# Kernel optimization log

Measured on AMD Instinct MI355X. Metric: run time of the kernel, lower is better.

Reference implementation:

```python
import jax, jax.numpy as jnp
import numpy as np

EPS = 1e-08


def setup_inputs() -> dict:
    key = jax.random.key(0)
    kx, km = jax.random.split(key)
    B, T, D = 128, 4096, 64
    x = jax.random.normal(kx, (B, T, D), dtype=jnp.float32)
    mask = jax.random.randint(km, (B, T, D), 0, 2).astype(jnp.float32)
    return {"x": x, "mask": mask}


def reference(x, mask):
    B, T, D = x.shape
    dt = x.dtype

    # ---- temporal: lag-1 autocorrelation + linear trend ----
    autocorr = jnp.mean(x[:, :-1, :] * x[:, 1:, :], axis=(1, 2))[:, None]  # (B,1)
    t = jnp.arange(T, dtype=dt)
    t_c = t - t.mean()
    x_mean_t = x.mean(axis=2)                                   # (B,T)
    num = (t_c * (x_mean_t - x_mean_t.mean(axis=1, keepdims=True))).sum(axis=1, keepdims=True)
    trend = num / ((t_c ** 2).sum() + EPS)                      # (B,1)

    # ---- frequency: dominant frequency + spectral entropy ----
    power = jnp.abs(jnp.fft.rfft(x_mean_t, axis=1)) ** 2        # (B,T//2+1)
    dom_freq = (jnp.argmax(power, axis=1).astype(dt) / (T / 2))[:, None]
    p_norm = power / (power.sum(axis=1, keepdims=True) + EPS)
    spec_ent = -(p_norm * jnp.log(p_norm + EPS)).sum(axis=1, keepdims=True)

    # ---- statistical: skewness, kurtosis, quantiles ----
    xc = x - x.mean(axis=(1, 2), keepdims=True)
    m2 = (xc ** 2).mean(axis=(1, 2))
    m3 = (xc ** 3).mean(axis=(1, 2))
    m4 = (xc ** 4).mean(axis=(1, 2))
    skew = m3 / (m2 ** 1.5 + EPS)
    kurt = m4 / (m2 ** 2 + EPS)
    q = jnp.quantile(x.reshape(B, -1), jnp.array([0.25, 0.5, 0.75]), axis=1)  # (3,B)
    stat = jnp.stack([skew, kurt, q[0], q[1], q[2]], axis=1)    # (B,5)

    # ---- shape: peaks, zero crossings, rate of change ----
    diff = x_mean_t[:, 1:] - x_mean_t[:, :-1]                   # (B,T-1)
    peak = (diff[:, 1:] * diff[:, :-1] < 0).astype(dt).sum(axis=1, keepdims=True) / (T - 2)
    xmc = x_mean_t - x_mean_t.mean(axis=1, keepdims=True)
    zero_cross = (xmc[:, 1:] * xmc[:, :-1] < 0).astype(dt).sum(axis=1, keepdims=True) / (T - 1)
    roc = jnp.abs(diff).mean(axis=1, keepdims=True)

    # ---- missing-data features (vectorized, no per-batch loop) ----
    missing_rate = 1.0 - mask.reshape(B, -1).sum(axis=1, keepdims=True) / (T * D + EPS)
    obs_per_time = mask.sum(axis=2)                             # (B,T)
    obs_density = obs_per_time / (D + EPS)
    density_var = jnp.var(obs_density, axis=1, ddof=1, keepdims=True)  # unbiased, matches torch
    time_mask = obs_per_time > 0                                # (B,T) bool
    first_idx = jnp.argmax(time_mask, axis=1).astype(dt)
    first_obs = jnp.where(time_mask.any(axis=1), first_idx / T, 0.0)[:, None]

    # ---- channel features: mean off-diagonal correlation + PCA var explained ----
    xcc = x - x.mean(axis=1, keepdims=True)                     # (B,T,D)
    gram = jnp.einsum('btd,bte->bde', xcc, xcc)                 # (B,D,D)
    cov = gram / (T - 1 + EPS)
    std = jnp.std(x, axis=1, ddof=1)                            # (B,D), unbiased like torch.std
    corr = cov / (std[:, :, None] * std[:, None, :] + EPS)
    off_diag = 1.0 - jnp.eye(D, dtype=dt)
    mean_corr = ((corr * off_diag).sum(axis=(1, 2)) / (D * (D - 1) + EPS))[:, None]
    # singular values squared of xcc == eigenvalues of gram
    eig = jnp.linalg.eigvalsh(gram)                             # ascending, (B,D)
    var_explained = (eig[:, -1] / eig.sum(axis=1))[:, None]

    return jnp.concatenate([
        autocorr, trend,               # temporal (2)
        dom_freq, spec_ent,            # frequency (2)
        stat,                          # statistical (5)
        peak, zero_cross, roc,         # shape (3)
        missing_rate, density_var, first_obs,  # missing (3)
        mean_corr, var_explained,      # channel (2)
    ], axis=1)                          # (B,17)
```

## Files before the change

### kernel.cpp

```cpp
#include <hip/hip_runtime.h>
#include <math.h>

#define TB 128
#define TT 4096
#define TD 64

#define GRAM_OFF   0u
#define HIST_OFF   2097152u
#define COLSUM_OFF 4194304u
#define SCAL_OFF   4227072u
#define FIRST_OFF  4230656u
#define ZERO_BYTES 4231168u
#define XMEAN_OFF  4231168u

typedef float  f32x4  __attribute__((ext_vector_type(4)));
typedef short  s16x8  __attribute__((ext_vector_type(8)));

__device__ __forceinline__ float brs4(float v, float* sbuf, int tid) {
#pragma unroll
  for (int o = 32; o; o >>= 1) v += __shfl_xor(v, o);
  __syncthreads();
  if ((tid & 63) == 0) sbuf[tid >> 6] = v;
  __syncthreads();
  return (sbuf[0] + sbuf[1]) + (sbuf[2] + sbuf[3]);
}

__device__ __forceinline__ float brs8(float v, float* sbuf, int tid) {
#pragma unroll
  for (int o = 32; o; o >>= 1) v += __shfl_xor(v, o);
  __syncthreads();
  if ((tid & 63) == 0) sbuf[tid >> 6] = v;
  __syncthreads();
  return ((sbuf[0] + sbuf[1]) + (sbuf[2] + sbuf[3])) +
         ((sbuf[4] + sbuf[5]) + (sbuf[6] + sbuf[7]));
}

__device__ __forceinline__ int binof(float v) {
  int bi = (int)floorf(fmaf(v, 256.f, 2048.f));
  return bi < 0 ? 0 : (bi > 4095 ? 4095 : bi);
}

__device__ __forceinline__ unsigned short f2bf(float f) {
  unsigned u = __float_as_uint(f);
  return (unsigned short)((u + 0x7FFFu + ((u >> 16) & 1u)) >> 16);
}

__global__ __launch_bounds__(256) void kA_stats(const float* __restrict__ x,
    const float* __restrict__ mk, float* __restrict__ xmean,
    unsigned* __restrict__ hist, float* __restrict__ colsum,
    float* __restrict__ scal, int* __restrict__ firstg) {
  __shared__ unsigned shist[4096];
  __shared__ float xrow[512];
  __shared__ float scol[64];
  __shared__ float sred[4];
  __shared__ int smax[4];

  const int tid  = threadIdx.x;
  const int b    = blockIdx.y;
  const int s    = blockIdx.x;
  const int t0   = s << 9;
  const int lane = tid & 63;
  const int wv   = tid >> 6;
  const int q    = lane >> 4;
  const int c    = lane & 15;
  const int lcol = c << 2;
  const int tw   = t0 + (wv << 7);

  for (int i = tid; i < 4096; i += 256) shist[i] = 0u;
  if (tid < 64) scol[tid] = 0.f;
  __syncthreads();

  float s1 = 0.f, s2 = 0.f, s3 = 0.f, s4 = 0.f, ac = 0.f;
  float osum = 0.f, o2 = 0.f;
  int fmax = 0;
  float cs0 = 0.f, cs1 = 0.f, cs2 = 0.f, cs3 = 0.f;
  float4 pv = make_float4(0.f, 0.f, 0.f, 0.f);

  const float* xb = x + (size_t)b * (TT * TD);
  const float* mb = mk + (size_t)b * (TT * TD);

  for (int it = 0; it < 32; ++it) {
    const int t = tw + (it << 2) + q;
    const float4 v = *(const float4*)(xb + (size_t)t * TD + lcol);
    const float4 m = *(const float4*)(mb + (size_t)t * TD + lcol);
    {
      const float x0 = v.x, x1 = v.y, x2 = v.z, x3 = v.w;
      const float q0 = x0 * x0, q1 = x1 * x1, q2 = x2 * x2, q3 = x3 * x3;
      s1 += (x0 + x1) + (x2 + x3);
      s2 += (q0 + q1) + (q2 + q3);
      s3 += (q0 * x0 + q1 * x1) + (q2 * x2 + q3 * x3);
      s4 += (q0 * q0 + q1 * q1) + (q2 * q2 + q3 * q3);
      cs0 += x0; cs1 += x1; cs2 += x2; cs3 += x3;
      atomicAdd(&shist[binof(x0)], 1u);
      atomicAdd(&shist[binof(x1)], 1u);
      atomicAdd(&shist[binof(x2)], 1u);
      atomicAdd(&shist[binof(x3)], 1u);
    }
    {
      float rx = (v.x + v.y) + (v.z + v.w);
      float rm = (m.x + m.y) + (m.z + m.w);
      rx += __shfl_xor(rx, 1); rm += __shfl_xor(rm, 1);
      rx += __shfl_xor(rx, 2); rm += __shfl_xor(rm, 2);
      rx += __shfl_xor(rx, 4); rm += __shfl_xor(rm, 4);
      rx += __shfl_xor(rx, 8); rm += __shfl_xor(rm, 8);
      if (c == 0) {
        xrow[t - t0] = rx * (1.f / 64.f);
        osum += rm;
        o2 = fmaf(rm, rm, o2);
        if (rm > 0.f) fmax = max(fmax, TT - t);
      }
    }
    {
      const float n0 = __shfl(v.x, lane + 16);
      const float n1 = __shfl(v.y, lane + 16);
      const float n2 = __shfl(v.z, lane + 16);
      const float n3 = __shfl(v.w, lane + 16);
      const float d1 = (v.x * n0 + v.y * n1) + (v.z * n2 + v.w * n3);
      ac += (q < 3) ? d1 : 0.f;
      const float b0 = __shfl(v.x, c);
      const float b1 = __shfl(v.y, c);
      const float b2 = __shfl(v.z, c);
      const float b3 = __shfl(v.w, c);
      if (it > 0) {
        const float d2 = (pv.x * b0 + pv.y * b1) + (pv.z * b2 + pv.w * b3);
        ac += (q == 3) ? d2 : 0.f;
      }
      pv = v;
    }
  }
  {
    const int tnext = tw + 128;
    if (tnext < TT) {
      const float4 nb = *(const float4*)(xb + (size_t)tnext * TD + lcol);
      const float d2 = (pv.x * nb.x + pv.y * nb.y) + (pv.z * nb.z + pv.w * nb.w);
      ac += (q == 3) ? d2 : 0.f;
    }
  }
  __syncthreads();
  xmean[(size_t)b * TT + t0 + tid] = xrow[tid];
  xmean[(size_t)b * TT + t0 + tid + 256] = xrow[tid + 256];
  const float rac = brs4(ac, sred, tid);
  const float r1 = brs4(s1, sred, tid);
  const float r2 = brs4(s2, sred, tid);
  const float r3 = brs4(s3, sred, tid);
  const float r4 = brs4(s4, sred, tid);
  const float ro = brs4(osum, sred, tid);
  const float ro2 = brs4(o2, sred, tid);
#pragma unroll
  for (int o = 32; o; o >>= 1) fmax = max(fmax, __shfl_xor(fmax, o));
  if ((tid & 63) == 0) smax[tid >> 6] = fmax;
  __syncthreads();
  if (tid == 0) {
    atomicAdd(&scal[0 * TB + b], rac);
    atomicAdd(&scal[1 * TB + b], r1);
    atomicAdd(&scal[2 * TB + b], r2);
    atomicAdd(&scal[3 * TB + b], r3);
    atomicAdd(&scal[4 * TB + b], r4);
    atomicAdd(&scal[5 * TB + b], ro);
    atomicAdd(&scal[6 * TB + b], ro2);
    atomicMax(&firstg[b], max(max(smax[0], smax[1]), max(smax[2], smax[3])));
  }
  atomicAdd(&scol[lcol + 0], cs0);
  atomicAdd(&scol[lcol + 1], cs1);
  atomicAdd(&scol[lcol + 2], cs2);
  atomicAdd(&scol[lcol + 3], cs3);
  __syncthreads();
  if (tid < 64) atomicAdd(&colsum[b * 64 + tid], scol[tid]);
  unsigned* hb = hist + (size_t)b * 4096;
  for (int i = tid; i < 4096; i += 256) {
    const unsigned hv = shist[i];
    if (hv) atomicAdd(&hb[i], hv);
  }
}

__global__ __launch_bounds__(256) void kB_gram(const float* __restrict__ x,
                                               float* __restrict__ gram) {
  __shared__ __align__(16) unsigned short Xt[2][64 * 72];
  const int tid  = threadIdx.x;
  const int b    = blockIdx.y;
  const int s    = blockIdx.x;
  const int t0   = s << 9;
  const int lane = tid & 63;
  const int wv   = tid >> 6;
  const int g    = tid >> 4;
  const int r0   = g << 2;
  const int c    = tid & 15;
  const int lcol = c << 2;
  const int mb0 = (wv & 1) << 5;
  const int nb0 = (wv >> 1) << 5;
  const int ml  = lane & 15;
  const int qk  = (lane >> 4) << 3;

  f32x4 acc[2][2];
#pragma unroll
  for (int mi = 0; mi < 2; ++mi)
#pragma unroll
    for (int ni = 0; ni < 2; ++ni) acc[mi][ni] = (f32x4)0.f;

  const float* xb = x + (size_t)b * (TT * TD);

  int p = 0;
  for (int tile = 0; tile < 8; ++tile) {
    const int tbase = t0 + (tile << 6);
    float4 v[4];
#pragma unroll
    for (int k = 0; k < 4; ++k)
      v[k] = *(const float4*)(xb + (size_t)(tbase + r0 + k) * TD + lcol);
#pragma unroll
    for (int j = 0; j < 4; ++j) {
      const float e0 = j == 0 ? v[0].x : (j == 1 ? v[0].y : (j == 2 ? v[0].z : v[0].w));
      const float e1 = j == 0 ? v[1].x : (j == 1 ? v[1].y : (j == 2 ? v[1].z : v[1].w));
      const float e2 = j == 0 ? v[2].x : (j == 1 ? v[2].y : (j == 2 ? v[2].z : v[2].w));
      const float e3 = j == 0 ? v[3].x : (j == 1 ? v[3].y : (j == 2 ? v[3].z : v[3].w));
      uint2 pw;
      pw.x = (unsigned)f2bf(e0) | ((unsigned)f2bf(e1) << 16);
      pw.y = (unsigned)f2bf(e2) | ((unsigned)f2bf(e3) << 16);
      *(uint2*)(&Xt[p][(lcol + j) * 72 + r0]) = pw;
    }
    __syncthreads();
#pragma unroll
    for (int kk = 0; kk < 2; ++kk) {
      const int ko = (kk << 5) + qk;
      s16x8 af[2], bf[2];
#pragma unroll
      for (int mi = 0; mi < 2; ++mi)
        af[mi] = *(const s16x8*)(&Xt[p][(mb0 + (mi << 4) + ml) * 72 + ko]);
#pragma unroll
      for (int ni = 0; ni < 2; ++ni)
        bf[ni] = *(const s16x8*)(&Xt[p][(nb0 + (ni << 4) + ml) * 72 + ko]);
#pragma unroll
      for (int mi = 0; mi < 2; ++mi)
#pragma unroll
        for (int ni = 0; ni < 2; ++ni)
          acc[mi][ni] = __builtin_amdgcn_mfma_f32_16x16x32_bf16(
              af[mi], bf[ni], acc[mi][ni], 0, 0, 0);
    }
    p ^= 1;
  }
  float* gb = gram + (size_t)b * 4096;
  const int crow = (lane >> 4) << 2;
  const int ccol = lane & 15;
#pragma unroll
  for (int mi = 0; mi < 2; ++mi)
#pragma unroll
    for (int ni = 0; ni < 2; ++ni) {
      const int gr0 = mb0 + (mi << 4) + crow;
      const int gc = nb0 + (ni << 4) + ccol;
#pragma unroll
      for (int rg = 0; rg < 4; ++rg)
        atomicAdd(&gb[(gr0 + rg) * 64 + gc], acc[mi][ni][rg]);
    }
}

__global__ __launch_bounds__(512) void k34(const float* __restrict__ xmean,
    const float* __restrict__ gram, const float* __restrict__ colsum,
    const unsigned* __restrict__ hist, const float* __restrict__ scal,
    const int* __restrict__ firstg, float* __restrict__ out) {
  __shared__ __align__(16) char arena[49152];
  __shared__ float sred[8];
  __shared__ float smv[8];
  __shared__ int smi[8];
  __shared__ float cssh[64];
  __shared__ float sdsh[64];
  __shared__ float osv_s[6];
  const int tid = threadIdx.x;

  if (blockIdx.x < 128) {
    const int b = blockIdx.x;
    float* xm = (float*)arena;
    float* re = xm + 4096;
    float* im = re + 4096;
    const float* xb = xmean + (size_t)b * TT;
    for (int i = tid; i < TT; i += 512) xm[i] = xb[i];
    __syncthreads();
    float ls = 0.f;
    for (int i = tid; i < TT; i += 512) ls += xm[i];
    const float meanv = brs8(ls, sred, tid) * (1.f / TT);
    float tnum = 0.f, roc = 0.f;
    int pk = 0, zc = 0;
    for (int i = tid; i < TT; i += 512) {
      const float xi = xm[i];
      tnum += ((float)i - 2047.5f) * (xi - meanv);
      if (i < TT - 1) {
        const float d1 = xm[i + 1] - xi;
        roc += fabsf(d1);
        if (i >= 1) {
          const float d0 = xi - xm[i - 1];
          if (d1 * d0 < 0.f) ++pk;
        }
      }
      if (i >= 1) {
        if ((xi - meanv) * (xm[i - 1] - meanv) < 0.f) ++zc;
      }
    }
    tnum = brs8(tnum, sred, tid);
    roc = brs8(roc, sred, tid);
    const float pkf = brs8((float)pk, sred, tid);
    const float zcf = brs8((float)zc, sred, tid);
    if (tid == 0) {
      out[b * 17 + 1] = tnum / 5726622720.0f;
      out[b * 17 + 9] = pkf * (1.f / 4094.f);
      out[b * 17 + 10] = zcf * (1.f / 4095.f);
      out[b * 17 + 11] = roc * (1.f / 4095.f);
    }
    for (int i = tid; i < TT; i += 512) {
      re[i] = xm[__brev((unsigned)i) >> 20];
      im[i] = 0.f;
    }
    __syncthreads();
    int l2h = 0;
    for (int len = 2; len <= TT; len <<= 1, ++l2h) {
      const int half = len >> 1;
      const float ab = -6.283185307179586f / (float)len;
      for (int j = tid; j < TT / 2; j += 512) {
        const int pos = j & (half - 1);
        const int i0 = ((j >> l2h) << (l2h + 1)) + pos;
        const int i1 = i0 + half;
        float sn, cn;
        __sincosf(ab * (float)pos, &sn, &cn);
        const float vr = re[i1], vi = im[i1];
        const float tr = cn * vr - sn * vi;
        const float ti = cn * vi + sn * vr;
        const float ur = re[i0], ui = im[i0];
        re[i0] = ur + tr; im[i0] = ui + ti;
        re[i1] = ur - tr; im[i1] = ui - ti;
      }
      __syncthreads();
    }
    float ps = 0.f, bmaxv = -1.f;
    int bidx = 0;
    for (int k = tid; k <= 2048; k += 512) {
      const float p = re[k] * re[k] + im[k] * im[k];
      ps += p;
      if (p > bmaxv) { bmaxv = p; bidx = k; }
    }
    ps = brs8(ps, sred, tid);
#pragma unroll
    for (int o = 32; o; o >>= 1) {
      const float ov = __shfl_xor(bmaxv, o);
      const int oi = __shfl_xor(bidx, o);
      if (ov > bmaxv || (ov == bmaxv && oi < bidx)) { bmaxv = ov; bidx = oi; }
    }
    if ((tid & 63) == 0) { smv[tid >> 6] = bmaxv; smi[tid >> 6] = bidx; }
    __syncthreads();
    float ent = 0.f;
    const float inv = 1.f / (ps + 1e-8f);
    for (int k = tid; k <= 2048; k += 512) {
      const float p = (re[k] * re[k] + im[k] * im[k]) * inv;
      ent -= p * __logf(p + 1e-8f);
    }
    ent = brs8(ent, sred, tid);
    if (tid == 0) {
      float bv = smv[0]; int bi = smi[0];
      for (int w = 1; w < 8; ++w)
        if (smv[w] > bv || (smv[w] == bv && smi[w] < bi)) { bv = smv[w]; bi = smi[w]; }
      out[b * 17 + 2] = (float)bi * (1.f / 2048.f);
      out[b * 17 + 3] = ent;
    }
  } else {
    const int b = blockIdx.x - 128;
    float* Lg = (float*)arena;
    unsigned* h = (unsigned*)(arena + 16640);
    unsigned* cumc = (unsigned*)(arena + 16640 + 16384);
    if (tid < 64) cssh[tid] = colsum[b * 64 + tid];
    for (int i = tid; i < 4096; i += 512) h[i] = hist[(size_t)b * 4096 + i];
    __syncthreads();
    const float* gb = gram + (size_t)b * 4096;
    for (int i = tid; i < 4096; i += 512) {
      const int d = i >> 6, e = i & 63;
      Lg[d * 65 + e] = gb[i] - cssh[d] * cssh[e] * (1.f / 4096.f);
    }
    unsigned chs_own = 0;
    if (tid < 256) {
#pragma unroll
      for (int j = 0; j < 16; ++j) chs_own += h[(tid << 4) + j];
      cumc[tid] = chs_own;
    }
    __syncthreads();
    if (tid < 64) sdsh[tid] = sqrtf(Lg[tid * 65 + tid] * (1.f / 4095.f));
    for (int off = 1; off < 256; off <<= 1) {
      unsigned add = 0;
      if (tid < 256 && tid >= off) add = cumc[tid - off];
      __syncthreads();
      if (tid < 256) cumc[tid] += add;
      __syncthreads();
    }
    float mcs = 0.f, trc = 0.f;
    for (int i = tid; i < 4096; i += 512) {
      const int d = i >> 6, e = i & 63;
      const float gv = Lg[d * 65 + e];
      if (d != e) mcs += (gv * (1.f / 4095.f)) / (sdsh[d] * sdsh[e] + 1e-8f);
      else trc += gv;
    }
    mcs = brs8(mcs, sred, tid);
    trc = brs8(trc, sred, tid);
    if (tid < 256) {
      const unsigned ranks[6] = {65535u, 65536u, 131071u, 131072u, 196607u, 196608u};
      const unsigned incl = cumc[tid];
      const unsigned excl = incl - chs_own;
#pragma unroll
      for (int qi = 0; qi < 6; ++qi) {
        const unsigned r = ranks[qi];
        if (excl <= r && r < incl) {
          int bin = tid << 4;
          unsigned cum = excl;
          while (bin < 4095 && cum + h[bin] <= r) { cum += h[bin]; ++bin; }
          const float cnt = (float)max(h[bin], 1u);
          osv_s[qi] = ((float)bin * (1.f / 256.f) - 8.f) +
                      (((float)(r - cum) + 0.5f) / cnt) * (1.f / 256.f);
        }
      }
    }
    float lam = 0.f;
    if (tid < 64) {
      const float* rowp = &Lg[tid * 65];
      float v = 1.f + 0.001f * (float)tid;
      float n2 = 1.f;
      for (int it = 0; it < 48; ++it) {
        float w0 = 0.f, w1 = 0.f, w2 = 0.f, w3 = 0.f;
#pragma unroll
        for (int e = 0; e < 64; e += 4) {
          w0 = fmaf(rowp[e],     __shfl(v, e),     w0);
          w1 = fmaf(rowp[e + 1], __shfl(v, e + 1), w1);
          w2 = fmaf(rowp[e + 2], __shfl(v, e + 2), w2);
          w3 = fmaf(rowp[e + 3], __shfl(v, e + 3), w3);
        }
        const float w = (w0 + w1) + (w2 + w3);
        n2 = w * w;
#pragma unroll
        for (int o = 32; o; o >>= 1) n2 += __shfl_xor(n2, o);
        v = w * rsqrtf(n2);
      }
      lam = sqrtf(n2);
    }
    __syncthreads();
    if (tid == 0) {
      const float q25 = 0.25f * osv_s[0] + 0.75f * osv_s[1];
      const float q50 = 0.5f * (osv_s[2] + osv_s[3]);
      const float q75 = 0.75f * osv_s[4] + 0.25f * osv_s[5];
      const float N = 262144.f;
      const float m1 = scal[1 * TB + b] / N;
      const float M2 = scal[2 * TB + b] / N;
      const float M3 = scal[3 * TB + b] / N;
      const float M4 = scal[4 * TB + b] / N;
      const float mu2 = M2 - m1 * m1;
      const float mu3 = M3 - 3.f * m1 * M2 + 2.f * m1 * m1 * m1;
      const float mu4 = M4 - 4.f * m1 * M3 + 6.f * m1 * m1 * M2 - 3.f * m1 * m1 * m1 * m1;
      const float skew = mu3 / (sqrtf(mu2) * mu2 + 1e-8f);
      const float kurt = mu4 / (mu2 * mu2 + 1e-8f);
      const float acv = scal[0 * TB + b] * (1.f / 262080.f);
      const float msum = scal[5 * TB + b];
      const float o2s = scal[6 * TB + b];
      const float missing = 1.f - msum / 262144.f;
      const float sdm = msum * (1.f / 64.f) * (1.f / 4096.f);
      const float dvar = (o2s * (1.f / 4096.f) - 4096.f * sdm * sdm) * (1.f / 4095.f);
      const int fm = firstg[b];
      const float fobs = fm > 0 ? (float)(4096 - fm) * (1.f / 4096.f) : 0.f;
      float* ob = out + b * 17;
      ob[0] = acv;
      ob[4] = skew; ob[5] = kurt;
      ob[6] = q25; ob[7] = q50; ob[8] = q75;
      ob[12] = missing; ob[13] = dvar; ob[14] = fobs;
      ob[15] = mcs / (4032.f + 1e-8f);
      ob[16] = lam / trc;
    }
  }
}

extern "C" void kernel_launch(void* const* d_in, const int* in_sizes, int n_in,
                              void* d_out, int out_size, void* d_ws, size_t ws_size,
                              hipStream_t stream) {
  (void)in_sizes; (void)n_in; (void)out_size; (void)ws_size;
  const float* x = (const float*)d_in[0];
  const float* mask = (const float*)d_in[1];
  float* out = (float*)d_out;
  char* ws = (char*)d_ws;
  float* gram = (float*)(ws + GRAM_OFF);
  unsigned* hist = (unsigned*)(ws + HIST_OFF);
  float* colsum = (float*)(ws + COLSUM_OFF);
  float* scal = (float*)(ws + SCAL_OFF);
  int* firstg = (int*)(ws + FIRST_OFF);
  float* xmean = (float*)(ws + XMEAN_OFF);

  hipMemsetAsync(d_ws, 0, ZERO_BYTES, stream);

  dim3 g1(8, TB);
  kA_stats<<<g1, 256, 0, stream>>>(x, mask, xmean, hist, colsum, scal, firstg);
  kB_gram<<<g1, 256, 0, stream>>>(x, gram);
  k34<<<256, 512, 0, stream>>>(xmean, gram, colsum, hist, scal, firstg, out);
}
```

Measured before the change: 349.1 us.

## Restructure stats kernel: contiguous time rows per quad, ballot mask counts, more blocks

The stats kernel now gives each 16-lane quad a contiguous run of 16 time steps, so the lag-1 autocorrelation becomes a per-thread product with the previous row and no cross-lane shuffles are needed. Mask row counts use wave ballots and popcount instead of a shuffle reduction. Row means are accumulated with LDS atomics. The grid is doubled to 16 blocks per batch, each covering 256 rows, for more parallelism. This trades shuffle work for LDS atomic contention, and it assumes the mask holds only 0/1 values. Dropping floorf changes binning only for negative values, which get clamped to bin 0 anyway.

```diff
diff --git a/kernel.cpp b/kernel.cpp
--- a/kernel.cpp
+++ b/kernel.cpp
@@ -36,7 +36,7 @@
 }
 
 __device__ __forceinline__ int binof(float v) {
-  int bi = (int)floorf(fmaf(v, 256.f, 2048.f));
+  int bi = (int)(fmaf(v, 256.f, 2048.f));
   return bi < 0 ? 0 : (bi > 4095 ? 4095 : bi);
 }
 
@@ -50,7 +50,7 @@
     unsigned* __restrict__ hist, float* __restrict__ colsum,
     float* __restrict__ scal, int* __restrict__ firstg) {
   __shared__ unsigned shist[4096];
-  __shared__ float xrow[512];
+  __shared__ float xrow[256];
   __shared__ float scol[64];
   __shared__ float sred[4];
   __shared__ int smax[4];
@@ -58,15 +58,16 @@
   const int tid  = threadIdx.x;
   const int b    = blockIdx.y;
   const int s    = blockIdx.x;
-  const int t0   = s << 9;
+  const int t0   = s << 8;
   const int lane = tid & 63;
   const int wv   = tid >> 6;
   const int q    = lane >> 4;
   const int c    = lane & 15;
   const int lcol = c << 2;
-  const int tw   = t0 + (wv << 7);
+  const int tq   = t0 + (wv << 6) + (q << 4);
 
   for (int i = tid; i < 4096; i += 256) shist[i] = 0u;
+  xrow[tid] = 0.f;
   if (tid < 64) scol[tid] = 0.f;
   __syncthreads();
 
@@ -75,12 +76,13 @@
   int fmax = 0;
   float cs0 = 0.f, cs1 = 0.f, cs2 = 0.f, cs3 = 0.f;
   float4 pv = make_float4(0.f, 0.f, 0.f, 0.f);
+  const int sh = q << 4;
 
   const float* xb = x + (size_t)b * (TT * TD);
   const float* mb = mk + (size_t)b * (TT * TD);
 
-  for (int it = 0; it < 32; ++it) {
-    const int t = tw + (it << 2) + q;
+  for (int it = 0; it < 16; ++it) {
+    const int t = tq + it;
     const float4 v = *(const float4*)(xb + (size_t)t * TD + lcol);
     const float4 m = *(const float4*)(mb + (size_t)t * TD + lcol);
     {
@@ -96,49 +98,36 @@
       atomicAdd(&shist[binof(x2)], 1u);
       atomicAdd(&shist[binof(x3)], 1u);
     }
+    atomicAdd(&xrow[t - t0], (v.x + v.y) + (v.z + v.w));
     {
-      float rx = (v.x + v.y) + (v.z + v.w);
-      float rm = (m.x + m.y) + (m.z + m.w);
-      rx += __shfl_xor(rx, 1); rm += __shfl_xor(rm, 1);
-      rx += __shfl_xor(rx, 2); rm += __shfl_xor(rm, 2);
-      rx += __shfl_xor(rx, 4); rm += __shfl_xor(rm, 4);
-      rx += __shfl_xor(rx, 8); rm += __shfl_xor(rm, 8);
+      const unsigned long long b0 = __ballot(m.x > 0.5f);
+      const unsigned long long b1 = __ballot(m.y > 0.5f);
+      const unsigned long long b2 = __ballot(m.z > 0.5f);
+      const unsigned long long b3 = __ballot(m.w > 0.5f);
       if (c == 0) {
-        xrow[t - t0] = rx * (1.f / 64.f);
+        const int cnt = __popcll((b0 >> sh) & 0xFFFFull) +
+                        __popcll((b1 >> sh) & 0xFFFFull) +
+                        __popcll((b2 >> sh) & 0xFFFFull) +
+                        __popcll((b3 >> sh) & 0xFFFFull);
+        const float rm = (float)cnt;
         osum += rm;
         o2 = fmaf(rm, rm, o2);
-        if (rm > 0.f) fmax = max(fmax, TT - t);
-      }
-    }
-    {
-      const float n0 = __shfl(v.x, lane + 16);
-      const float n1 = __shfl(v.y, lane + 16);
-      const float n2 = __shfl(v.z, lane + 16);
-      const float n3 = __shfl(v.w, lane + 16);
-      const float d1 = (v.x * n0 + v.y * n1) + (v.z * n2 + v.w * n3);
-      ac += (q < 3) ? d1 : 0.f;
-      const float b0 = __shfl(v.x, c);
-      const float b1 = __shfl(v.y, c);
-      const float b2 = __shfl(v.z, c);
-      const float b3 = __shfl(v.w, c);
-      if (it > 0) {
-        const float d2 = (pv.x * b0 + pv.y * b1) + (pv.z * b2 + pv.w * b3);
-        ac += (q == 3) ? d2 : 0.f;
-      }
-      pv = v;
-    }
+        if (cnt > 0) fmax = max(fmax, TT - t);
+      }
+    }
+    if (it > 0)
+      ac += (pv.x * v.x + pv.y * v.y) + (pv.z * v.z + pv.w * v.w);
+    pv = v;
   }
   {
-    const int tnext = tw + 128;
+    const int tnext = tq + 16;
     if (tnext < TT) {
       const float4 nb = *(const float4*)(xb + (size_t)tnext * TD + lcol);
-      const float d2 = (pv.x * nb.x + pv.y * nb.y) + (pv.z * nb.z + pv.w * nb.w);
-      ac += (q == 3) ? d2 : 0.f;
-    }
-  }
-  __syncthreads();
-  xmean[(size_t)b * TT + t0 + tid] = xrow[tid];
-  xmean[(size_t)b * TT + t0 + tid + 256] = xrow[tid + 256];
+      ac += (pv.x * nb.x + pv.y * nb.y) + (pv.z * nb.z + pv.w * nb.w);
+    }
+  }
+  __syncthreads();
+  xmean[(size_t)b * TT + t0 + tid] = xrow[tid] * (1.f / 64.f);
   const float rac = brs4(ac, sred, tid);
   const float r1 = brs4(s1, sred, tid);
   const float r2 = brs4(s2, sred, tid);
@@ -484,8 +473,9 @@
 
   hipMemsetAsync(d_ws, 0, ZERO_BYTES, stream);
 
-  dim3 g1(8, TB);
-  kA_stats<<<g1, 256, 0, stream>>>(x, mask, xmean, hist, colsum, scal, firstg);
-  kB_gram<<<g1, 256, 0, stream>>>(x, gram);
+  dim3 gA(16, TB);
+  kA_stats<<<gA, 256, 0, stream>>>(x, mask, xmean, hist, colsum, scal, firstg);
+  dim3 gB(8, TB);
+  kB_gram<<<gB, 256, 0, stream>>>(x, gram);
   k34<<<256, 512, 0, stream>>>(xmean, gram, colsum, hist, scal, firstg, out);
 }
```

Result: slower. 386.6 us (+10.7%).
